# Kernel optimization log

Hardware: AMD Instinct MI355X
Metric: run time of the kernel (lower is better)

Reference implementation:

```python
import jax, jax.numpy as jnp
import numpy as np

ALPHA = 1.0
NUM_SEGMENTS = 50000  # number of structures (segments)


def setup_inputs() -> dict:
    key = jax.random.key(0)
    k1, k2, k3 = jax.random.split(key, 3)
    n, d = 1000000, 128
    prop = jax.random.normal(k1, (1, n, d), dtype=jnp.float32)
    weights = jax.random.uniform(k2, (1, n), dtype=jnp.float32)
    index = jnp.sort(jax.random.randint(k3, (1, n), 0, NUM_SEGMENTS, dtype=jnp.int32))
    return {"prop": prop, "weights": weights, "index": index}


def reference(prop, weights, index):
    # result_s = sum_{i in segment s} w_i^alpha * prop_i / sum_{i in s} w_i^alpha
    expo_w = weights ** ALPHA                      # [1, n]
    idx = index.reshape(-1)                        # [n]
    weighted = prop * expo_w[:, :, None]           # [1, n, d]
    prop_sum = jax.ops.segment_sum(weighted[0], idx, num_segments=NUM_SEGMENTS)[None]   # [1, S, d]
    weight_sum = jax.ops.segment_sum(expo_w[0], idx, num_segments=NUM_SEGMENTS)[None]   # [1, S]
    return prop_sum / weight_sum[:, :, None]
```

## Files before the change

kernel.cpp:

```cpp
#include <hip/hip_runtime.h>
#include <hip/hip_bf16.h>

#define NUM_SEGMENTS 50000

__global__ void build_starts(const int* __restrict__ idx,
                             int* __restrict__ starts,
                             int n, int S) {
    int i = blockIdx.x * blockDim.x + threadIdx.x;
    if (i >= n) return;
    int cur = idx[i];
    if (i == 0) {
        for (int s = 0; s <= cur; ++s) starts[s] = 0;
    } else {
        int prev = idx[i - 1];
        for (int s = prev + 1; s <= cur; ++s) starts[s] = i;
    }
    if (i == n - 1) {
        for (int s = cur + 1; s <= S; ++s) starts[s] = n;
    }
}

__global__ void __launch_bounds__(128)
seg_weighted_avg_d128(const float4* __restrict__ prop4,
                      const float*  __restrict__ w,
                      const int*    __restrict__ starts,
                      float4*       __restrict__ out4) {
    const int s     = blockIdx.x;
    const int start = starts[s];
    const int nrows = starts[s + 1] - start;

    const int t    = threadIdx.x;
    const int col4 = t & 31;
    const int rg   = t >> 5;

    const float4* p = prop4 + (size_t)(start + rg) * 32 + col4;
    const float*  wp = w + start;

    float4 acc = make_float4(0.f, 0.f, 0.f, 0.f);
    float wsum = 0.0f;

    int r = rg;
    for (; r + 4 < nrows; r += 8) {
        float  w0 = wp[r],        w1 = wp[r + 4];
        float4 p0 = p[0],         p1 = p[128];
        p += 256;
        acc.x = fmaf(w0, p0.x, acc.x); acc.y = fmaf(w0, p0.y, acc.y);
        acc.z = fmaf(w0, p0.z, acc.z); acc.w = fmaf(w0, p0.w, acc.w);
        acc.x = fmaf(w1, p1.x, acc.x); acc.y = fmaf(w1, p1.y, acc.y);
        acc.z = fmaf(w1, p1.z, acc.z); acc.w = fmaf(w1, p1.w, acc.w);
        wsum += w0 + w1;
    }
    for (; r < nrows; r += 4) {
        float  w0 = wp[r];
        float4 p0 = p[0];
        p += 128;
        acc.x = fmaf(w0, p0.x, acc.x); acc.y = fmaf(w0, p0.y, acc.y);
        acc.z = fmaf(w0, p0.z, acc.z); acc.w = fmaf(w0, p0.w, acc.w);
        wsum += w0;
    }

    __shared__ float4 lacc[128];
    __shared__ float  lw[128];
    lacc[t] = acc;
    lw[t]   = wsum;
    __syncthreads();

    if (t < 32) {
        float4 a0 = lacc[t], a1 = lacc[t + 32], a2 = lacc[t + 64], a3 = lacc[t + 96];
        float ws = (lw[t] + lw[t + 32]) + (lw[t + 64] + lw[t + 96]);
        float4 res;
        res.x = ((a0.x + a1.x) + (a2.x + a3.x)) / ws;
        res.y = ((a0.y + a1.y) + (a2.y + a3.y)) / ws;
        res.z = ((a0.z + a1.z) + (a2.z + a3.z)) / ws;
        res.w = ((a0.w + a1.w) + (a2.w + a3.w)) / ws;
        out4[(size_t)s * 32 + t] = res;
    }
}

__global__ void __launch_bounds__(128)
seg_weighted_avg_generic(const float* __restrict__ prop,
                         const float* __restrict__ w,
                         const int*   __restrict__ starts,
                         float*       __restrict__ out,
                         int d) {
    const int s     = blockIdx.x;
    const int start = starts[s];
    const int end   = starts[s + 1];
    const int t     = threadIdx.x;
    const float* p  = prop + (size_t)start * d + t;
    float acc = 0.f, wsum = 0.f;
    for (int i = start; i < end; ++i) {
        float wi = w[i];
        wsum += wi;
        acc = fmaf(wi, p[0], acc);
        p += d;
    }
    out[(size_t)s * d + t] = acc / wsum;
}

extern "C" void kernel_launch(void* const* d_in, const int* in_sizes, int n_in,
                              void* d_out, int out_size, void* d_ws, size_t ws_size,
                              hipStream_t stream) {
    const float* prop = (const float*)d_in[0];
    const float* w    = (const float*)d_in[1];
    const int*   idx  = (const int*)d_in[2];
    float* out        = (float*)d_out;

    const int n = in_sizes[1];
    const int d = in_sizes[0] / in_sizes[1];
    const int S = NUM_SEGMENTS;

    int* starts = (int*)d_ws;

    build_starts<<<(n + 255) / 256, 256, 0, stream>>>(idx, starts, n, S);

    if (d == 128) {
        seg_weighted_avg_d128<<<S, 128, 0, stream>>>(
            (const float4*)prop, w, starts, (float4*)out);
    } else {
        seg_weighted_avg_generic<<<S, d, 0, stream>>>(prop, w, starts, out, d);
    }
}
```

Baseline: 106.5 us.

## Process two segments per block, use nontemporal loads/stores, vectorize start-index build

The main kernel now handles two consecutive segments per 128-thread block, halving the grid and sharing the starts lookup and the shared-memory reduction between them. Prop reads and output writes use nontemporal builtins so the streamed data bypasses cache retention. The starts-building kernel reads the index as int4, so each thread covers four rows. The two segments are processed one after the other within a block, so per-block latency grows and parallelism drops; odd S falls back to the slow generic kernel.

Result: faster. 96.53 us (-9.3%).

```diff
diff --git a/kernel.cpp b/kernel.cpp
--- a/kernel.cpp
+++ b/kernel.cpp
@@ -3,77 +3,104 @@
 
 #define NUM_SEGMENTS 50000
 
-__global__ void build_starts(const int* __restrict__ idx,
-                             int* __restrict__ starts,
-                             int n, int S) {
-    int i = blockIdx.x * blockDim.x + threadIdx.x;
+typedef float f32x4 __attribute__((ext_vector_type(4)));
+
+__device__ __forceinline__ f32x4 ntload4(const f32x4* p) {
+    return __builtin_nontemporal_load(p);
+}
+__device__ __forceinline__ void ntstore4(f32x4* p, f32x4 v) {
+    __builtin_nontemporal_store(v, p);
+}
+
+__global__ void build_starts_v4(const int4* __restrict__ idx4,
+                                const int*  __restrict__ idx,
+                                int* __restrict__ starts,
+                                int n4, int n, int S) {
+    int i4 = blockIdx.x * blockDim.x + threadIdx.x;
+    if (i4 >= n4) return;
+    int4 v = idx4[i4];
+    int base = i4 * 4;
+    int prev = (base == 0) ? -1 : idx[base - 1];
+    int a0 = v.x, a1 = v.y, a2 = v.z, a3 = v.w;
+    for (int s = prev + 1; s <= a0; ++s) starts[s] = base;
+    for (int s = a0 + 1;  s <= a1; ++s) starts[s] = base + 1;
+    for (int s = a1 + 1;  s <= a2; ++s) starts[s] = base + 2;
+    for (int s = a2 + 1;  s <= a3; ++s) starts[s] = base + 3;
+    if (base + 4 >= n) {
+        for (int s = a3 + 1; s <= S; ++s) starts[s] = n;
+    }
+}
+
+__global__ void build_starts_tail(const int* __restrict__ idx,
+                                  int* __restrict__ starts,
+                                  int n4, int n, int S) {
+    int i = n4 * 4 + blockIdx.x * blockDim.x + threadIdx.x;
     if (i >= n) return;
     int cur = idx[i];
-    if (i == 0) {
-        for (int s = 0; s <= cur; ++s) starts[s] = 0;
-    } else {
-        int prev = idx[i - 1];
-        for (int s = prev + 1; s <= cur; ++s) starts[s] = i;
+    int prev = (i == 0) ? -1 : idx[i - 1];
+    for (int s = prev + 1; s <= cur; ++s) starts[s] = i;
+    if (i == n - 1)
+        for (int s = cur + 1; s <= S; ++s) starts[s] = n;
+}
+
+__device__ __forceinline__ void accum_seg(const f32x4* __restrict__ prop4,
+                                          const float* __restrict__ w,
+                                          int start, int nrows,
+                                          int col4, int rg,
+                                          f32x4& acc, float& wsum) {
+    const f32x4* p  = prop4 + (size_t)(start + rg) * 32 + col4;
+    const float* wp = w + start;
+    int r = rg;
+    for (; r + 4 < nrows; r += 8) {
+        float w0 = wp[r], w1 = wp[r + 4];
+        f32x4 p0 = ntload4(p), p1 = ntload4(p + 128);
+        p += 256;
+        acc += p0 * w0;
+        acc += p1 * w1;
+        wsum += w0 + w1;
     }
-    if (i == n - 1) {
-        for (int s = cur + 1; s <= S; ++s) starts[s] = n;
+    for (; r < nrows; r += 4) {
+        float w0 = wp[r];
+        f32x4 p0 = ntload4(p);
+        p += 128;
+        acc += p0 * w0;
+        wsum += w0;
     }
 }
 
 __global__ void __launch_bounds__(128)
-seg_weighted_avg_d128(const float4* __restrict__ prop4,
-                      const float*  __restrict__ w,
-                      const int*    __restrict__ starts,
-                      float4*       __restrict__ out4) {
-    const int s     = blockIdx.x;
-    const int start = starts[s];
-    const int nrows = starts[s + 1] - start;
+seg_weighted_avg_d128(const f32x4* __restrict__ prop4,
+                      const float* __restrict__ w,
+                      const int*   __restrict__ starts,
+                      f32x4*       __restrict__ out4) {
+    const int s0  = blockIdx.x * 2;
+    const int st0 = starts[s0];
+    const int st1 = starts[s0 + 1];
+    const int st2 = starts[s0 + 2];
 
     const int t    = threadIdx.x;
     const int col4 = t & 31;
     const int rg   = t >> 5;
 
-    const float4* p = prop4 + (size_t)(start + rg) * 32 + col4;
-    const float*  wp = w + start;
+    f32x4 accA = (f32x4)0.f, accB = (f32x4)0.f;
+    float wsA = 0.f, wsB = 0.f;
 
-    float4 acc = make_float4(0.f, 0.f, 0.f, 0.f);
-    float wsum = 0.0f;
+    accum_seg(prop4, w, st0, st1 - st0, col4, rg, accA, wsA);
+    accum_seg(prop4, w, st1, st2 - st1, col4, rg, accB, wsB);
 
-    int r = rg;
-    for (; r + 4 < nrows; r += 8) {
-        float  w0 = wp[r],        w1 = wp[r + 4];
-        float4 p0 = p[0],         p1 = p[128];
-        p += 256;
-        acc.x = fmaf(w0, p0.x, acc.x); acc.y = fmaf(w0, p0.y, acc.y);
-        acc.z = fmaf(w0, p0.z, acc.z); acc.w = fmaf(w0, p0.w, acc.w);
-        acc.x = fmaf(w1, p1.x, acc.x); acc.y = fmaf(w1, p1.y, acc.y);
-        acc.z = fmaf(w1, p1.z, acc.z); acc.w = fmaf(w1, p1.w, acc.w);
-        wsum += w0 + w1;
-    }
-    for (; r < nrows; r += 4) {
-        float  w0 = wp[r];
-        float4 p0 = p[0];
-        p += 128;
-        acc.x = fmaf(w0, p0.x, acc.x); acc.y = fmaf(w0, p0.y, acc.y);
-        acc.z = fmaf(w0, p0.z, acc.z); acc.w = fmaf(w0, p0.w, acc.w);
-        wsum += w0;
-    }
-
-    __shared__ float4 lacc[128];
-    __shared__ float  lw[128];
-    lacc[t] = acc;
-    lw[t]   = wsum;
+    __shared__ f32x4 laccA[128], laccB[128];
+    __shared__ float lwA[128], lwB[128];
+    laccA[t] = accA; laccB[t] = accB;
+    lwA[t]   = wsA;  lwB[t]   = wsB;
     __syncthreads();
 
-    if (t < 32) {
-        float4 a0 = lacc[t], a1 = lacc[t + 32], a2 = lacc[t + 64], a3 = lacc[t + 96];
-        float ws = (lw[t] + lw[t + 32]) + (lw[t + 64] + lw[t + 96]);
-        float4 res;
-        res.x = ((a0.x + a1.x) + (a2.x + a3.x)) / ws;
-        res.y = ((a0.y + a1.y) + (a2.y + a3.y)) / ws;
-        res.z = ((a0.z + a1.z) + (a2.z + a3.z)) / ws;
-        res.w = ((a0.w + a1.w) + (a2.w + a3.w)) / ws;
-        out4[(size_t)s * 32 + t] = res;
+    if (t < 64) {
+        const f32x4* lacc = (t < 32) ? laccA : laccB;
+        const float* lw   = (t < 32) ? lwA   : lwB;
+        const int u = t & 31;
+        f32x4 a = (lacc[u] + lacc[u + 32]) + (lacc[u + 64] + lacc[u + 96]);
+        float ws = (lw[u] + lw[u + 32]) + (lw[u + 64] + lw[u + 96]);
+        ntstore4((f32x4*)&out4[(size_t)(s0 + (t >> 5)) * 32 + u], a / ws);
     }
 }
 
@@ -112,11 +139,17 @@
 
     int* starts = (int*)d_ws;
 
-    build_starts<<<(n + 255) / 256, 256, 0, stream>>>(idx, starts, n, S);
+    const int n4 = n / 4;
+    build_starts_v4<<<(n4 + 255) / 256, 256, 0, stream>>>(
+        (const int4*)idx, idx, starts, n4, n, S);
+    if (n % 4) {
+        build_starts_tail<<<((n - n4 * 4) + 255) / 256, 256, 0, stream>>>(
+            idx, starts, n4, n, S);
+    }
 
-    if (d == 128) {
-        seg_weighted_avg_d128<<<S, 128, 0, stream>>>(
-            (const float4*)prop, w, starts, (float4*)out);
+    if (d == 128 && (S % 2) == 0) {
+        seg_weighted_avg_d128<<<S / 2, 128, 0, stream>>>(
+            (const f32x4*)prop, w, starts, (f32x4*)out);
     } else {
         seg_weighted_avg_generic<<<S, d, 0, stream>>>(prop, w, starts, out, d);
     }
```
